# Optimization experiments

Measured on AMD Instinct MI355X. Metric: run time of the kernel, lower is better.

## Reference

```python
import jax, jax.numpy as jnp
import numpy as np

NUM_CLASSES = 80
FOCAL_ALPHA = 0.25
FOCAL_GAMMA = 2.0
HUBER_SIGMA = 3.0
REG_MEAN = 0.0
REG_STD = 0.2
IMG_H = 800.0
IMG_W = 800.0
B, A, M = 4, 100000, 32


def setup_inputs() -> dict:
    key = jax.random.key(0)
    k1, k2, k3, k4, k5, k6, k7 = jax.random.split(key, 7)
    classification = jax.random.uniform(k1, (B, A, NUM_CLASSES), dtype=jnp.float32)
    regression = jax.random.normal(k2, (B, A, 4), dtype=jnp.float32)
    # plausible anchors: centers inside image, sizes 16..256
    cx = jax.random.uniform(k3, (A,), minval=0.0, maxval=IMG_W)
    cy = jax.random.uniform(k4, (A,), minval=0.0, maxval=IMG_H)
    s = jax.random.uniform(k5, (A, 2), minval=16.0, maxval=256.0)
    anchors = jnp.stack([cx - s[:, 0] / 2, cy - s[:, 1] / 2,
                         cx + s[:, 0] / 2, cy + s[:, 1] / 2], axis=1).astype(jnp.float32)
    # annotations: [B, M, 5] = x1,y1,x2,y2,class
    xy = jax.random.uniform(k6, (B, M, 2), minval=0.0, maxval=650.0)
    wh = jax.random.uniform(k7, (B, M, 2), minval=30.0, maxval=150.0)
    cls = jax.random.randint(jax.random.fold_in(key, 9), (B, M, 1), 0, NUM_CLASSES).astype(jnp.float32)
    annotations = jnp.concatenate([xy, xy + wh, cls], axis=-1)
    return {"classification": classification, "regression": regression,
            "anchors": anchors, "annotations": annotations}


def _pairwise_iou(anchors, boxes):
    # anchors [A,4], boxes [M,4] -> [A,M]
    ix1 = jnp.maximum(anchors[:, None, 0], boxes[None, :, 0])
    iy1 = jnp.maximum(anchors[:, None, 1], boxes[None, :, 1])
    ix2 = jnp.minimum(anchors[:, None, 2], boxes[None, :, 2])
    iy2 = jnp.minimum(anchors[:, None, 3], boxes[None, :, 3])
    inter = jnp.clip(ix2 - ix1, 0.0) * jnp.clip(iy2 - iy1, 0.0)
    area_a = (anchors[:, 2] - anchors[:, 0]) * (anchors[:, 3] - anchors[:, 1])
    area_b = (boxes[:, 2] - boxes[:, 0]) * (boxes[:, 3] - boxes[:, 1])
    union = area_a[:, None] + area_b[None, :] - inter
    return inter / jnp.maximum(union, 1e-8)


def _targets(anchors, annotations):
    # per-image anchor assignment, vmapped over batch
    def per_image(ann):
        boxes = ann[:, :4]
        cls = ann[:, 4].astype(jnp.int32)
        ious = _pairwise_iou(anchors, boxes)          # [A,M]
        best = jnp.argmax(ious, axis=1)               # [A]
        best_iou = jnp.max(ious, axis=1)
        pos = best_iou >= 0.5
        ign = (best_iou > 0.4) & (~pos)
        states = jnp.where(pos, 1.0, jnp.where(ign, -1.0, 0.0))
        cx = (anchors[:, 0] + anchors[:, 2]) * 0.5
        cy = (anchors[:, 1] + anchors[:, 3]) * 0.5
        inside = (cx >= 0) & (cx < IMG_W) & (cy >= 0) & (cy < IMG_H)
        states = jnp.where(inside, states, -1.0)
        labels = jax.nn.one_hot(cls[best], NUM_CLASSES, dtype=jnp.float32) * pos[:, None]
        ab = boxes[best]                              # assigned gt boxes [A,4]
        aw = anchors[:, 2] - anchors[:, 0]
        ah = anchors[:, 3] - anchors[:, 1]
        t = jnp.stack([(ab[:, 0] - anchors[:, 0]) / aw,
                       (ab[:, 1] - anchors[:, 1]) / ah,
                       (ab[:, 2] - anchors[:, 2]) / aw,
                       (ab[:, 3] - anchors[:, 3]) / ah], axis=1)
        t = (t - REG_MEAN) / REG_STD
        return labels, t, states
    return jax.vmap(per_image)(annotations)


def reference(classification, regression, anchors, annotations):
    labels, reg_t, states = _targets(anchors, annotations)   # [B,A,K],[B,A,4],[B,A]
    num_pos = jnp.maximum(jnp.sum((states == 1.0).astype(jnp.float32)), 1.0)
    # focal loss over non-ignored anchors
    valid = (states != -1.0)[..., None].astype(jnp.float32)
    p = jnp.clip(classification, 1e-4, 1.0 - 1e-4)
    bce = -(labels * jnp.log(p) + (1.0 - labels) * jnp.log1p(-p))
    alpha_f = jnp.where(labels == 1.0, FOCAL_ALPHA, 1.0 - FOCAL_ALPHA)
    focal_w = alpha_f * jnp.where(labels == 1.0, 1.0 - p, p) ** FOCAL_GAMMA
    cls_loss = jnp.sum(focal_w * bce * valid) / num_pos
    # smooth L1 over positive anchors
    pos_m = (states == 1.0)[..., None].astype(jnp.float32)
    s2 = HUBER_SIGMA ** 2
    d = jnp.abs(regression - reg_t)
    l1 = jnp.where(d < 1.0 / s2, 0.5 * s2 * d * d, d - 0.5 / s2)
    reg_loss = jnp.sum(l1 * pos_m) / num_pos
    return cls_loss + reg_loss
```

## Files before the change

kernel.cpp:

```cpp
#include <hip/hip_runtime.h>

#define BB 4
#define AA 100000
#define MM 32
#define NC 80
#define GX 391
#define NBLK (GX * BB)
#define FB 3125
#define FT (FB * 256)
#define N4 (BB * AA * (NC/4))
#define LN2 0.69314718055994530942f


__device__ __forceinline__ float hw_log2(float x) {
#if defined(__has_builtin)
#if __has_builtin(__builtin_amdgcn_logf)
    return __builtin_amdgcn_logf(x);
#else
    return __log2f(x);
#endif
#else
    return __log2f(x);
#endif
}

__device__ __forceinline__ float clampp(float p) {
    return fminf(fmaxf(p, 1e-4f), 0.9999f);
}
__device__ __forceinline__ float fneg(float p) {
    return 0.75f * p * p * (-LN2 * hw_log2(1.0f - p));
}
__device__ __forceinline__ float fpos(float p) {
    const float q = 1.0f - p;
    return 0.25f * q * q * (-LN2 * hw_log2(p));
}

__global__ __launch_bounds__(256) void targets_kernel(
    const float* __restrict__ anchors,
    const float* __restrict__ annotations,
    const float* __restrict__ regression,
    const float* __restrict__ cls,
    float* __restrict__ reg_part,
    unsigned* __restrict__ pos_part)
{
    __shared__ float ann[MM * 5];
    const int b = blockIdx.y;
    const int tid = threadIdx.x;
    if (tid < MM * 5) ann[tid] = annotations[b * MM * 5 + tid];
    __syncthreads();

    const int a = blockIdx.x * 256 + tid;
    float acc = 0.0f;
    int pos_cnt = 0;

    if (a < AA) {
        const float4 an = ((const float4*)anchors)[a];
        const float ax1 = an.x, ay1 = an.y, ax2 = an.z, ay2 = an.w;
        const float area_a = __fmul_rn(__fsub_rn(ax2, ax1), __fsub_rn(ay2, ay1));

        float best_iou = -1.0f;
        int best = 0;
        #pragma unroll
        for (int j = 0; j < MM; ++j) {
            const float bx1 = ann[j * 5 + 0];
            const float by1 = ann[j * 5 + 1];
            const float bx2 = ann[j * 5 + 2];
            const float by2 = ann[j * 5 + 3];
            const float ix1 = fmaxf(ax1, bx1);
            const float iy1 = fmaxf(ay1, by1);
            const float ix2 = fminf(ax2, bx2);
            const float iy2 = fminf(ay2, by2);
            const float iw = fmaxf(__fsub_rn(ix2, ix1), 0.0f);
            const float ih = fmaxf(__fsub_rn(iy2, iy1), 0.0f);
            const float inter = __fmul_rn(iw, ih);
            const float area_b = __fmul_rn(__fsub_rn(bx2, bx1), __fsub_rn(by2, by1));
            const float uni = __fsub_rn(__fadd_rn(area_a, area_b), inter);
            const float iou = __fdiv_rn(inter, fmaxf(uni, 1e-8f));
            if (iou > best_iou) { best_iou = iou; best = j; }
        }

        const bool pos = best_iou >= 0.5f;
        const bool ign = (best_iou > 0.4f) && !pos;
        const float cx = (ax1 + ax2) * 0.5f;
        const float cy = (ay1 + ay2) * 0.5f;
        const bool inside = (cx >= 0.0f) && (cx < 800.0f) && (cy >= 0.0f) && (cy < 800.0f);

        int code = -2;
        if (inside && !ign) code = pos ? (int)ann[best * 5 + 4] : -1;

        if (pos && inside) {
            pos_cnt = 1;
            const float aw = ax2 - ax1;
            const float ah = ay2 - ay1;
            const float bx1 = ann[best * 5 + 0];
            const float by1 = ann[best * 5 + 1];
            const float bx2 = ann[best * 5 + 2];
            const float by2 = ann[best * 5 + 3];
            float t[4];
            t[0] = ((bx1 - ax1) / aw) / 0.2f;
            t[1] = ((by1 - ay1) / ah) / 0.2f;
            t[2] = ((bx2 - ax2) / aw) / 0.2f;
            t[3] = ((by2 - ay2) / ah) / 0.2f;
            const float* rg = regression + (((size_t)b * AA + a) * 4);
            #pragma unroll
            for (int k = 0; k < 4; ++k) {
                const float d = fabsf(rg[k] - t[k]);
                acc += (d < (1.0f / 9.0f)) ? (4.5f * d * d) : (d - (0.5f / 9.0f));
            }
        }

        if (code == -2) {
            const float4* c4 = (const float4*)cls + ((size_t)b * AA + a) * 20;
            #pragma unroll 4
            for (int k = 0; k < 20; ++k) {
                const float4 v = c4[k];
                acc -= fneg(clampp(v.x)) + fneg(clampp(v.y))
                     + fneg(clampp(v.z)) + fneg(clampp(v.w));
            }
        } else if (code >= 0) {
            const float p = clampp(cls[((size_t)b * AA + a) * NC + code]);
            acc += fpos(p) - fneg(p);
        }
    }

    #pragma unroll
    for (int off = 32; off > 0; off >>= 1) {
        acc     += __shfl_down(acc, off);
        pos_cnt += __shfl_down(pos_cnt, off);
    }
    __shared__ float wr[4];
    __shared__ int   wp[4];
    const int wave = tid >> 6, lane = tid & 63;
    if (lane == 0) { wr[wave] = acc; wp[wave] = pos_cnt; }
    __syncthreads();
    if (tid == 0) {
        const int idx = b * GX + blockIdx.x;
        reg_part[idx] = wr[0] + wr[1] + wr[2] + wr[3];
        pos_part[idx] = (unsigned)(wp[0] + wp[1] + wp[2] + wp[3]);
    }
}

__global__ __launch_bounds__(256) void focal_kernel(
    const float4* __restrict__ cls4,
    float* __restrict__ cls_part)
{
    const int t0 = blockIdx.x * 256 + threadIdx.x;
    float4 v[10];
    #pragma unroll
    for (int k = 0; k < 10; ++k) v[k] = cls4[t0 + k * FT];
    __builtin_amdgcn_sched_barrier(0);

    float s0 = 0.0f, s1 = 0.0f, s2 = 0.0f, s3 = 0.0f;
    #pragma unroll
    for (int k = 0; k < 10; ++k) {
        const float p0 = clampp(v[k].x);
        const float p1 = clampp(v[k].y);
        const float p2 = clampp(v[k].z);
        const float p3 = clampp(v[k].w);
        s0 -= p0 * p0 * hw_log2(1.0f - p0);
        s1 -= p1 * p1 * hw_log2(1.0f - p1);
        s2 -= p2 * p2 * hw_log2(1.0f - p2);
        s3 -= p3 * p3 * hw_log2(1.0f - p3);
    }
    float csum = (0.75f * LN2) * ((s0 + s1) + (s2 + s3));

    #pragma unroll
    for (int off = 32; off > 0; off >>= 1) csum += __shfl_down(csum, off);
    __shared__ float wc[4];
    const int wave = threadIdx.x >> 6, lane = threadIdx.x & 63;
    if (lane == 0) wc[wave] = csum;
    __syncthreads();
    if (threadIdx.x == 0) cls_part[blockIdx.x] = wc[0] + wc[1] + wc[2] + wc[3];
}

__global__ __launch_bounds__(256) void finalize_kernel(
    const float* __restrict__ reg_part,
    const unsigned* __restrict__ pos_part,
    const float* __restrict__ cls_part,
    float* __restrict__ out)
{
    float cs = 0.0f, rs = 0.0f;
    unsigned pc = 0;
    for (int i = threadIdx.x; i < FB; i += 256) cs += cls_part[i];
    for (int i = threadIdx.x; i < NBLK; i += 256) { rs += reg_part[i]; pc += pos_part[i]; }
    #pragma unroll
    for (int off = 32; off > 0; off >>= 1) {
        cs += __shfl_down(cs, off);
        rs += __shfl_down(rs, off);
        pc += __shfl_down(pc, off);
    }
    __shared__ float wc[4], wr[4];
    __shared__ unsigned wp[4];
    const int wave = threadIdx.x >> 6, lane = threadIdx.x & 63;
    if (lane == 0) { wc[wave] = cs; wr[wave] = rs; wp[wave] = pc; }
    __syncthreads();
    if (threadIdx.x == 0) {
        const float csum = wc[0] + wc[1] + wc[2] + wc[3];
        const float rsum = wr[0] + wr[1] + wr[2] + wr[3];
        const float np = fmaxf((float)(wp[0] + wp[1] + wp[2] + wp[3]), 1.0f);
        out[0] = (csum + rsum) / np;
    }
}

extern "C" void kernel_launch(void* const* d_in, const int* in_sizes, int n_in,
                              void* d_out, int out_size, void* d_ws, size_t ws_size,
                              hipStream_t stream)
{
    const float* classification = (const float*)d_in[0];
    const float* regression     = (const float*)d_in[1];
    const float* anchors        = (const float*)d_in[2];
    const float* annotations    = (const float*)d_in[3];
    float* out = (float*)d_out;

    float*    reg_part = (float*)d_ws;
    unsigned* pos_part = (unsigned*)d_ws + NBLK;
    float*    cls_part = (float*)d_ws + 2 * NBLK;

    focal_kernel<<<FB, 256, 0, stream>>>((const float4*)classification, cls_part);
    dim3 gA(GX, BB);
    targets_kernel<<<gA, 256, 0, stream>>>(anchors, annotations, regression,
                                           classification, reg_part, pos_part);
    finalize_kernel<<<1, 256, 0, stream>>>(reg_part, pos_part, cls_part, out);
}
```

Measured before the change: 216.8 us.

## Cooperatively load excluded anchor rows across wavefront and reorder kernel launches

In the targets kernel, the per-thread strided 80-float loop over outside-image anchors becomes a ballot loop. The whole wavefront reads each such anchor's row coalesced and reduces it with shuffles, so uncoalesced per-thread row reads are replaced by contiguous accesses. The focal kernel no longer preloads all ten float4 values ahead of a sched barrier and instead loads them inside the compute loop. The targets kernel now launches before the focal kernel, possibly to change cache residency of classification data. Serial per-row iterations and less explicit memory-level parallelism are the tradeoff.

```diff
diff --git a/kernel.cpp b/kernel.cpp
--- a/kernel.cpp
+++ b/kernel.cpp
@@ -52,6 +52,7 @@
     const int a = blockIdx.x * 256 + tid;
     float acc = 0.0f;
     int pos_cnt = 0;
+    int code = -3;
 
     if (a < AA) {
         const float4 an = ((const float4*)anchors)[a];
@@ -85,7 +86,7 @@
         const float cy = (ay1 + ay2) * 0.5f;
         const bool inside = (cx >= 0.0f) && (cx < 800.0f) && (cy >= 0.0f) && (cy < 800.0f);
 
-        int code = -2;
+        code = -2;
         if (inside && !ign) code = pos ? (int)ann[best * 5 + 4] : -1;
 
         if (pos && inside) {
@@ -108,19 +109,26 @@
                 acc += (d < (1.0f / 9.0f)) ? (4.5f * d * d) : (d - (0.5f / 9.0f));
             }
         }
-
-        if (code == -2) {
-            const float4* c4 = (const float4*)cls + ((size_t)b * AA + a) * 20;
-            #pragma unroll 4
-            for (int k = 0; k < 20; ++k) {
-                const float4 v = c4[k];
-                acc -= fneg(clampp(v.x)) + fneg(clampp(v.y))
-                     + fneg(clampp(v.z)) + fneg(clampp(v.w));
-            }
-        } else if (code >= 0) {
-            const float p = clampp(cls[((size_t)b * AA + a) * NC + code]);
-            acc += fpos(p) - fneg(p);
-        }
+    }
+
+    const int lane = tid & 63;
+
+    if (code >= 0) {
+        const float p = clampp(cls[(size_t)(b * AA + a) * NC + code]);
+        acc += fpos(p) - fneg(p);
+    }
+
+    unsigned long long exm = __ballot(code == -2);
+    while (exm) {
+        const int src = __builtin_ctzll(exm);
+        exm &= exm - 1;
+        const int eg = __shfl(b * AA + a, src);
+        const float* cb = cls + (size_t)eg * NC;
+        float x = fneg(clampp(cb[lane]));
+        if (lane < NC - 64) x += fneg(clampp(cb[64 + lane]));
+        #pragma unroll
+        for (int off = 32; off > 0; off >>= 1) x += __shfl_down(x, off);
+        if (lane == 0) acc -= x;
     }
 
     #pragma unroll
@@ -130,7 +138,7 @@
     }
     __shared__ float wr[4];
     __shared__ int   wp[4];
-    const int wave = tid >> 6, lane = tid & 63;
+    const int wave = tid >> 6;
     if (lane == 0) { wr[wave] = acc; wp[wave] = pos_cnt; }
     __syncthreads();
     if (tid == 0) {
@@ -145,18 +153,14 @@
     float* __restrict__ cls_part)
 {
     const int t0 = blockIdx.x * 256 + threadIdx.x;
-    float4 v[10];
-    #pragma unroll
-    for (int k = 0; k < 10; ++k) v[k] = cls4[t0 + k * FT];
-    __builtin_amdgcn_sched_barrier(0);
-
     float s0 = 0.0f, s1 = 0.0f, s2 = 0.0f, s3 = 0.0f;
     #pragma unroll
     for (int k = 0; k < 10; ++k) {
-        const float p0 = clampp(v[k].x);
-        const float p1 = clampp(v[k].y);
-        const float p2 = clampp(v[k].z);
-        const float p3 = clampp(v[k].w);
+        const float4 v = cls4[t0 + k * FT];
+        const float p0 = clampp(v.x);
+        const float p1 = clampp(v.y);
+        const float p2 = clampp(v.z);
+        const float p3 = clampp(v.w);
         s0 -= p0 * p0 * hw_log2(1.0f - p0);
         s1 -= p1 * p1 * hw_log2(1.0f - p1);
         s2 -= p2 * p2 * hw_log2(1.0f - p2);
@@ -216,9 +220,9 @@
     unsigned* pos_part = (unsigned*)d_ws + NBLK;
     float*    cls_part = (float*)d_ws + 2 * NBLK;
 
-    focal_kernel<<<FB, 256, 0, stream>>>((const float4*)classification, cls_part);
     dim3 gA(GX, BB);
     targets_kernel<<<gA, 256, 0, stream>>>(anchors, annotations, regression,
                                            classification, reg_part, pos_part);
+    focal_kernel<<<FB, 256, 0, stream>>>((const float4*)classification, cls_part);
     finalize_kernel<<<1, 256, 0, stream>>>(reg_part, pos_part, cls_part, out);
 }
```

New measurement: 216.9 us. About the same (+0.1%).
